# Kernel optimization log

Measured on AMD Instinct MI355X. Metric: run time of the kernel, lower is better.

Reference implementation:

```python
import jax, jax.numpy as jnp
import numpy as np

N_HEADS = 16
N_KV_HEADS = 8
N_REP = 2
HEAD_DIM = 128
SOFTCAP = 50.0
NEG_INF = -2.3819763e38
ROPE_BASE = 10000.0


def _rotate_half(x):
    x1, x2 = jnp.split(x, 2, axis=-1)
    return jnp.concatenate((-x2, x1), axis=-1)


def _rope_cos_sin(seq_len, dtype):
    # Gemma2RotaryEmbedding: inv_freq over even dims, emb = cat(freqs, freqs)
    inv_freq = 1.0 / (ROPE_BASE ** (jnp.arange(0, HEAD_DIM, 2, dtype=jnp.float32) / HEAD_DIM))
    freqs = jnp.arange(seq_len, dtype=jnp.float32)[:, None] * inv_freq[None, :]  # [s, hd/2]
    emb = jnp.concatenate((freqs, freqs), axis=-1)  # [s, hd]
    return jnp.cos(emb).astype(dtype), jnp.sin(emb).astype(dtype)


def setup_inputs() -> dict:
    key = jax.random.key(0)
    ks = jax.random.split(key, 5)
    b, s, d = 2, 2048, 2048
    w_scale = 0.02
    return {
        "x": jax.random.normal(ks[0], (b, s, d), dtype=jnp.float32),
        "wq": jax.random.normal(ks[1], (N_HEADS * HEAD_DIM, d), dtype=jnp.float32) * w_scale,
        "wk": jax.random.normal(ks[2], (N_KV_HEADS * HEAD_DIM, d), dtype=jnp.float32) * w_scale,
        "wv": jax.random.normal(ks[3], (N_KV_HEADS * HEAD_DIM, d), dtype=jnp.float32) * w_scale,
        "wo": jax.random.normal(ks[4], (d, N_HEADS * HEAD_DIM), dtype=jnp.float32) * w_scale,
    }


def reference(x, wq, wk, wv, wo):
    b, s, d = x.shape
    # QKV projections (linear_fn = plain x @ W.T)
    xq = (x @ wq.T).reshape(b, s, N_HEADS, HEAD_DIM).transpose(0, 2, 1, 3)      # [b,h,s,hd]
    xk = (x @ wk.T).reshape(b, s, N_KV_HEADS, HEAD_DIM).transpose(0, 2, 1, 3)   # [b,kv,s,hd]
    xv = (x @ wv.T).reshape(b, s, N_KV_HEADS, HEAD_DIM).transpose(0, 2, 1, 3)
    # Gemma2 rotary on q, k
    cos, sin = _rope_cos_sin(s, x.dtype)  # [s,hd] each, broadcast over b,h
    xq = xq * cos + _rotate_half(xq) * sin
    xk = xk * cos + _rotate_half(xk) * sin
    # repeat_kv: expand kv heads to n_heads
    keys = jnp.repeat(xk, N_REP, axis=1)
    values = jnp.repeat(xv, N_REP, axis=1)
    # scores with scaling and Gemma2 logit softcapping
    scale = float(HEAD_DIM) ** -0.5
    scores = jnp.einsum("bhsd,bhtd->bhst", xq * scale, keys)
    scores = jnp.tanh(scores / SOFTCAP) * SOFTCAP
    # causal additive mask [s, t]
    q_pos = jnp.arange(s)[:, None]
    k_pos = jnp.arange(s)[None, :]
    mask = jnp.where(k_pos <= q_pos, 0.0, NEG_INF).astype(jnp.float32)
    scores = scores + mask  # broadcast over [b,h]
    probs = jax.nn.softmax(scores.astype(jnp.float32), axis=-1).astype(xq.dtype)
    out = jnp.einsum("bhst,bhtd->bhsd", probs, values)
    out = out.transpose(0, 2, 1, 3).reshape(b, s, N_HEADS * HEAD_DIM)
    return out @ wo.T
```

## Files before the change

### kernel.cpp

```cpp
#include <hip/hip_runtime.h>
#include <stdint.h>
#include <stddef.h>

#define S_LEN   2048
#define DMODEL  2048
#define NHEADS  16
#define NKVH    8
#define HD      128
#define QPRE 1.7677669529663688e-3f
#define C1 72.13475204444817f

typedef __attribute__((ext_vector_type(8))) short  short8;
typedef __attribute__((ext_vector_type(4))) float  float4v;

static __device__ __forceinline__ unsigned short f2bf(float f) {
  union { float f; unsigned int u; } v; v.f = f;
  unsigned int u = v.u;
  u += 0x7fffu + ((u >> 16) & 1u);
  return (unsigned short)(u >> 16);
}
static __device__ __forceinline__ float bf2f(unsigned short b) {
  union { unsigned int u; float f; } v; v.u = ((unsigned int)b) << 16;
  return v.f;
}
static __device__ __forceinline__ void gload_lds16(const void* g, void* l) {
  __builtin_amdgcn_global_load_lds(
      (const __attribute__((address_space(1))) void*)g,
      (__attribute__((address_space(3))) void*)l, 16, 0, 0);
}

__global__ __launch_bounds__(256) void cvt_all(
    const float* __restrict__ x,  const float* __restrict__ wq,
    const float* __restrict__ wk, const float* __restrict__ wv,
    const float* __restrict__ wo,
    ushort4* __restrict__ xb, ushort4* __restrict__ wcat,
    ushort4* __restrict__ wob) {
  int i = blockIdx.x * 256 + threadIdx.x;
  const float4* src; ushort4* dst; int j;
  if (i < 2097152)      { src = (const float4*)x;  dst = xb;             j = i; }
  else if (i < 3145728) { src = (const float4*)wq; dst = wcat;           j = i - 2097152; }
  else if (i < 3670016) { src = (const float4*)wk; dst = wcat + 1048576; j = i - 3145728; }
  else if (i < 4194304) { src = (const float4*)wv; dst = wcat + 1572864; j = i - 3670016; }
  else                  { src = (const float4*)wo; dst = wob;            j = i - 4194304; }
  float4 v = src[j];
  ushort4 o;
  o.x = f2bf(v.x); o.y = f2bf(v.y); o.z = f2bf(v.z); o.w = f2bf(v.w);
  dst[j] = o;
}

__global__ __launch_bounds__(256, 2) void gemm_bf16(
    const unsigned short* __restrict__ A,
    const unsigned short* __restrict__ B,
    void* __restrict__ Cout, int N, int mode) {
  const int t    = threadIdx.x;
  const int lane = t & 63;
  const int w    = t >> 6;
  const int l15  = lane & 15;
  const int quad = lane >> 4;
  const int m0   = blockIdx.y * 128;
  const int n0   = blockIdx.x * 128;
  const int wm   = (w >> 1) * 64;
  const int wn   = (w & 1) * 64;

  __shared__ unsigned short At[128 * 32];
  __shared__ unsigned short Bt[128 * 32];

  float4v acc[4][4];
#pragma unroll
  for (int mt = 0; mt < 4; ++mt)
#pragma unroll
    for (int nt = 0; nt < 4; ++nt)
      acc[mt][nt] = (float4v){0.f, 0.f, 0.f, 0.f};

  const unsigned short* Abase = A + (size_t)m0 * DMODEL;
  const unsigned short* Bbase = B + (size_t)n0 * DMODEL;
  const int srow = w * 16 + (lane >> 2);
  const int sch  = (lane & 3) * 8;

  for (int k0 = 0; k0 < DMODEL; k0 += 32) {
#pragma unroll
    for (int r = 0; r < 2; ++r) {
      gload_lds16(Abase + (size_t)(r * 64 + srow) * DMODEL + k0 + sch,
                  At + (r * 256 + w * 64) * 8);
      gload_lds16(Bbase + (size_t)(r * 64 + srow) * DMODEL + k0 + sch,
                  Bt + (r * 256 + w * 64) * 8);
    }
    __syncthreads();
    short8 af[4], bf[4];
#pragma unroll
    for (int mt = 0; mt < 4; ++mt)
      af[mt] = *(const short8*)(At + (wm + mt * 16 + l15) * 32 + quad * 8);
#pragma unroll
    for (int nt = 0; nt < 4; ++nt)
      bf[nt] = *(const short8*)(Bt + (wn + nt * 16 + l15) * 32 + quad * 8);
#pragma unroll
    for (int mt = 0; mt < 4; ++mt)
#pragma unroll
      for (int nt = 0; nt < 4; ++nt)
        acc[mt][nt] = __builtin_amdgcn_mfma_f32_16x16x32_bf16(
            af[mt], bf[nt], acc[mt][nt], 0, 0, 0);
    __syncthreads();
  }

  float* C = (float*)Cout;
#pragma unroll
  for (int mt = 0; mt < 4; ++mt) {
    int row = m0 + wm + mt * 16 + quad * 4;
#pragma unroll
    for (int nt = 0; nt < 4; ++nt) {
      int col = n0 + wn + nt * 16 + l15;
#pragma unroll
      for (int r2 = 0; r2 < 4; ++r2)
        C[(size_t)(row + r2) * N + col] = acc[mt][nt][r2];
    }
  }
}

__global__ __launch_bounds__(512, 2) void gemm256_qkv(
    const unsigned short* __restrict__ A,
    const unsigned short* __restrict__ B,
    unsigned short* __restrict__ C) {
  const int t    = threadIdx.x;
  const int lane = t & 63;
  const int w    = t >> 6;
  const int l15  = lane & 15;
  const int quad = lane >> 4;

  const int id  = blockIdx.x;
  const int swz = (id & 7) * 32 + (id >> 3);
  const int m0  = (swz >> 4) * 256;
  const int n0  = (swz & 15) * 256;

  __shared__ unsigned short sm[2][2][2][128 * 64];

  const int wm  = w >> 2;
  const int wnq = w & 3;
  const int hB  = wnq >> 1;
  const int wnl = (wnq & 1) * 64;

  int soff[2];
#pragma unroll
  for (int i = 0; i < 2; ++i) {
    int P = (w * 2 + i) * 64 + lane;
    int r = P >> 3;
    int lc = (P & 7) ^ (r & 7);
    soff[i] = r * DMODEL + lc * 8;
  }
  const unsigned short* Ab = A + (size_t)m0 * DMODEL;
  const unsigned short* Bb = B + (size_t)n0 * DMODEL;

  auto stage = [&](int mat, int half, int buf, int kt) {
    const unsigned short* g =
        (mat ? Bb : Ab) + (size_t)half * 128 * DMODEL + kt * 64;
    unsigned short* l = &sm[buf][mat][half][(w * 2) * 512];
#pragma unroll
    for (int i = 0; i < 2; ++i)
      gload_lds16(g + soff[i], l + i * 512);
  };

  float4v acc[2][2][4][2];
#pragma unroll
  for (int qm = 0; qm < 2; ++qm)
#pragma unroll
    for (int qn = 0; qn < 2; ++qn)
#pragma unroll
      for (int mt = 0; mt < 4; ++mt)
#pragma unroll
        for (int nt = 0; nt < 2; ++nt)
          acc[qm][qn][mt][nt] = (float4v){0.f, 0.f, 0.f, 0.f};

  stage(0, 0, 0, 0); stage(0, 1, 0, 0); stage(1, 0, 0, 0); stage(1, 1, 0, 0);
  stage(0, 0, 1, 1); stage(0, 1, 1, 1); stage(1, 0, 1, 1);
  asm volatile("s_waitcnt vmcnt(6)" ::: "memory");
  __builtin_amdgcn_s_barrier();

  const int NT = DMODEL / 64;
#pragma unroll 1
  for (int j = 0; j < NT; ++j) {
    const int c = j & 1;
    const unsigned short* As = &sm[c][0][wm][0];
    const unsigned short* Bs = &sm[c][1][hB][0];
    short8 af[4][2], bf0[2][2], bf1[2][2];

#pragma unroll
    for (int mt = 0; mt < 4; ++mt)
#pragma unroll
      for (int kk = 0; kk < 2; ++kk) {
        int r = mt * 16 + l15;
        af[mt][kk] = *(const short8*)&As[r * 64 + (((kk * 4 + quad) ^ (r & 7)) * 8)];
      }
#pragma unroll
    for (int nt = 0; nt < 2; ++nt)
#pragma unroll
      for (int kk = 0; kk < 2; ++kk) {
        int r = wnl + nt * 16 + l15;
        bf0[nt][kk] = *(const short8*)&Bs[r * 64 + (((kk * 4 + quad) ^ (r & 7)) * 8)];
      }
    if (j + 1 < NT) stage(1, 1, c ^ 1, j + 1);
    __builtin_amdgcn_s_barrier();
    __builtin_amdgcn_s_setprio(1);
#pragma unroll
    for (int mt = 0; mt < 4; ++mt)
#pragma unroll
      for (int nt = 0; nt < 2; ++nt)
#pragma unroll
        for (int kk = 0; kk < 2; ++kk)
          acc[0][0][mt][nt] = __builtin_amdgcn_mfma_f32_16x16x32_bf16(
              af[mt][kk], bf0[nt][kk], acc[0][0][mt][nt], 0, 0, 0);
    __builtin_amdgcn_s_setprio(0);
    __builtin_amdgcn_s_barrier();

#pragma unroll
    for (int nt = 0; nt < 2; ++nt)
#pragma unroll
      for (int kk = 0; kk < 2; ++kk) {
        int r = wnl + 32 + nt * 16 + l15;
        bf1[nt][kk] = *(const short8*)&Bs[r * 64 + (((kk * 4 + quad) ^ (r & 7)) * 8)];
      }
    __builtin_amdgcn_s_barrier();
    __builtin_amdgcn_s_setprio(1);
#pragma unroll
    for (int mt = 0; mt < 4; ++mt)
#pragma unroll
      for (int nt = 0; nt < 2; ++nt)
#pragma unroll
        for (int kk = 0; kk < 2; ++kk)
          acc[0][1][mt][nt] = __builtin_amdgcn_mfma_f32_16x16x32_bf16(
              af[mt][kk], bf1[nt][kk], acc[0][1][mt][nt], 0, 0, 0);
    __builtin_amdgcn_s_setprio(0);
    __builtin_amdgcn_s_barrier();

#pragma unroll
    for (int mt = 0; mt < 4; ++mt)
#pragma unroll
      for (int kk = 0; kk < 2; ++kk) {
        int r = 64 + mt * 16 + l15;
        af[mt][kk] = *(const short8*)&As[r * 64 + (((kk * 4 + quad) ^ (r & 7)) * 8)];
      }
    __builtin_amdgcn_s_barrier();
    __builtin_amdgcn_s_setprio(1);
#pragma unroll
    for (int mt = 0; mt < 4; ++mt)
#pragma unroll
      for (int nt = 0; nt < 2; ++nt)
#pragma unroll
        for (int kk = 0; kk < 2; ++kk)
          acc[1][0][mt][nt] = __builtin_amdgcn_mfma_f32_16x16x32_bf16(
              af[mt][kk], bf0[nt][kk], acc[1][0][mt][nt], 0, 0, 0);
    __builtin_amdgcn_s_setprio(0);
    __builtin_amdgcn_s_barrier();

    if (j + 2 < NT) {
      stage(0, 0, c, j + 2); stage(0, 1, c, j + 2); stage(1, 0, c, j + 2);
    }
    __builtin_amdgcn_s_barrier();
    __builtin_amdgcn_s_setprio(1);
#pragma unroll
    for (int mt = 0; mt < 4; ++mt)
#pragma unroll
      for (int nt = 0; nt < 2; ++nt)
#pragma unroll
        for (int kk = 0; kk < 2; ++kk)
          acc[1][1][mt][nt] = __builtin_amdgcn_mfma_f32_16x16x32_bf16(
              af[mt][kk], bf1[nt][kk], acc[1][1][mt][nt], 0, 0, 0);
    __builtin_amdgcn_s_setprio(0);
    if (j + 2 < NT)      { asm volatile("s_waitcnt vmcnt(6)" ::: "memory"); }
    else if (j + 1 < NT) { asm volatile("s_waitcnt vmcnt(0)" ::: "memory"); }
    __builtin_amdgcn_s_barrier();
  }

#pragma unroll
  for (int qm = 0; qm < 2; ++qm)
#pragma unroll
    for (int mt = 0; mt < 4; ++mt) {
      int row0 = m0 + wm * 128 + qm * 64 + mt * 16 + quad * 4;
      int b = row0 >> 11, s0 = row0 & (S_LEN - 1);
#pragma unroll
      for (int qn = 0; qn < 2; ++qn)
#pragma unroll
        for (int nt = 0; nt < 2; ++nt) {
          int col = n0 + wnq * 64 + qn * 32 + nt * 16 + l15;
          float4v v = acc[qm][qn][mt][nt];
          if (col < 2048) {
            int head = col >> 7, d = col & (HD - 1);
#pragma unroll
            for (int r2 = 0; r2 < 4; ++r2)
              C[((size_t)(b * 16 + head) * S_LEN + s0 + r2) * HD + d] = f2bf(v[r2]);
          } else if (col < 3072) {
            int c2 = col - 2048;
            int kvh = c2 >> 7, d = c2 & (HD - 1);
#pragma unroll
            for (int r2 = 0; r2 < 4; ++r2)
              C[8388608 + ((size_t)(b * 8 + kvh) * S_LEN + s0 + r2) * HD + d] = f2bf(v[r2]);
          } else {
            int c2 = col - 3072;
            int kvh = c2 >> 7, d = c2 & (HD - 1);
            ushort4 pk;
            pk.x = f2bf(v[0]); pk.y = f2bf(v[1]);
            pk.z = f2bf(v[2]); pk.w = f2bf(v[3]);
            *(ushort4*)&C[12582912 + ((size_t)(b * 8 + kvh) * HD + d) * S_LEN + s0] = pk;
          }
        }
    }
}

__global__ __launch_bounds__(256) void rope_kernel(unsigned short* __restrict__ Q,
                                                   unsigned short* __restrict__ Kc) {
  int gt = blockIdx.x * 256 + threadIdx.x;
  int r = gt >> 6;
  int j = gt & 63;
  const int QROWS = 2 * NHEADS * S_LEN;
  bool isQ = (r < QROWS);
  unsigned short* p = isQ ? (Q + (size_t)r * HD)
                          : (Kc + (size_t)(r - QROWS) * HD);
  int pos = r & (S_LEN - 1);
  float inv = exp2f(-(float)j * 0.20762050593046868f);
  float ang = (float)pos * inv;
  float c = cosf(ang), s = sinf(ang);
  float sc = isQ ? QPRE : 1.0f;
  float x1 = bf2f(p[j]), x2 = bf2f(p[j + 64]);
  p[j]      = f2bf((x1 * c - x2 * s) * sc);
  p[j + 64] = f2bf((x2 * c + x1 * s) * sc);
}

__global__ __launch_bounds__(256, 2) void attn_kernel(
    const unsigned short* __restrict__ Q,
    const unsigned short* __restrict__ Kc,
    const unsigned short* __restrict__ Vt,
    unsigned short* __restrict__ Aout) {
  const int t    = threadIdx.x;
  const int lane = t & 63;
  const int w    = t >> 6;
  const int l15  = lane & 15;
  const int quad = lane >> 4;
  const int bh = blockIdx.x;
  const int pp = blockIdx.y;
  const int b = bh >> 4, h = bh & 15, kv = h >> 1;
  const int qtA = pp, qtB = 31 - pp;
  const int q0A = qtA * 64, q0B = qtB * 64;
  const int ntB = qtB + 1;

  __shared__ unsigned short Kt[2][64 * 128];
  __shared__ unsigned short Vts[2][128 * 64];
  __shared__ unsigned short Pt[4 * 2 * 1024];

  int offK[4], offV[4];
#pragma unroll
  for (int i = 0; i < 4; ++i) {
    int g = i * 256 + t;
    int rK = g >> 4, cK = (g & 15) ^ (rK & 7);
    offK[i] = rK * HD + cK * 8;
    int rV = g >> 3, cV = (g & 7) ^ (rV & 7);
    offV[i] = rV * S_LEN + cV * 8;
  }

  const unsigned short* QA = Q + ((size_t)(b * NHEADS + h) * S_LEN + q0A + w * 16) * HD;
  const unsigned short* QB = Q + ((size_t)(b * NHEADS + h) * S_LEN + q0B + w * 16) * HD;
  short8 qfA[4], qfB[4];
#pragma unroll
  for (int kk = 0; kk < 4; ++kk) {
    qfA[kk] = *(const short8*)&QA[l15 * HD + kk * 32 + quad * 8];
    qfB[kk] = *(const short8*)&QB[l15 * HD + kk * 32 + quad * 8];
  }

  float4v oA[8], oB[8];
#pragma unroll
  for (int nth = 0; nth < 8; ++nth) {
    oA[nth] = (float4v){0.f, 0.f, 0.f, 0.f};
    oB[nth] = (float4v){0.f, 0.f, 0.f, 0.f};
  }
  float lsA = 0.f, lsB = 0.f;

  const unsigned short* kg0 = Kc + (size_t)(b * NKVH + kv) * S_LEN * HD;
  const unsigned short* vg0 = Vt + (size_t)(b * NKVH + kv) * HD * S_LEN;
  unsigned short* PB = Pt + (w * 2 + 0) * 1024;
  unsigned short* PA = Pt + (w * 2 + 1) * 1024;

  auto stage = [&](int kt, int buf) {
    const unsigned short* kgp = kg0 + (size_t)kt * 64 * HD;
    const unsigned short* vgp = vg0 + (size_t)kt * 64;
#pragma unroll
    for (int i = 0; i < 4; ++i)
      gload_lds16(kgp + offK[i], &Kt[buf][(i * 256 + w * 64) * 8]);
#pragma unroll
    for (int i = 0; i < 4; ++i)
      gload_lds16(vgp + offV[i], &Vts[buf][(i * 256 + w * 64) * 8]);
  };

  auto softcap = [&](float x) -> float {
    float xx = __builtin_amdgcn_fmed3f(x, -0.26f, 0.26f);
    float x2 = xx * xx;
    float u = __builtin_fmaf(0.13333334f, x2, -0.33333334f);
    float v = __builtin_fmaf(u, x2, 1.0f);
    return __builtin_amdgcn_exp2f((C1 * xx) * v);
  };

  stage(0, 0);
  for (int kt = 0; kt < ntB; ++kt) {
    const int cur = kt & 1;
    __syncthreads();
    if (kt + 1 < ntB) stage(kt + 1, cur ^ 1);
    const bool doA   = (kt <= qtA);
    const bool diagA = (kt == qtA);
    const bool diagB = (kt == qtB);
    const unsigned short* Kb = Kt[cur];
    const unsigned short* Vb = Vts[cur];

#pragma unroll
    for (int ntk = 0; ntk < 4; ++ntk) {
      int pb = l15 * 64 + (((ntk * 2 + (quad >> 1)) ^ (l15 & 7)) * 8) + (quad & 1) * 4;
      short8 kf[4];
#pragma unroll
      for (int kk = 0; kk < 4; ++kk)
        kf[kk] = *(const short8*)
            &Kb[(ntk * 16 + l15) * HD + (((kk * 4 + quad) ^ (l15 & 7)) * 8)];

      if (diagB && (ntk * 16 > w * 16 + 15)) {
        uint2 z; z.x = 0u; z.y = 0u;
        *(uint2*)&PB[pb] = z;
      } else {
        float4v s0 = (float4v){0.f, 0.f, 0.f, 0.f};
#pragma unroll
        for (int kk = 0; kk < 4; ++kk)
          s0 = __builtin_amdgcn_mfma_f32_16x16x32_bf16(kf[kk], qfB[kk], s0, 0, 0, 0);
        float pv[4];
#pragma unroll
        for (int r = 0; r < 4; ++r) {
          float p = softcap(s0[r]);
          if (diagB)
            p = (ntk * 16 + quad * 4 + r <= w * 16 + l15) ? p : 0.f;
          lsB += p;
          pv[r] = p;
        }
        union { float f; unsigned u; } u0, u1, u2, u3;
        u0.f = pv[0]; u1.f = pv[1]; u2.f = pv[2]; u3.f = pv[3];
        uint2 pk;
        pk.x = __builtin_amdgcn_perm(u1.u, u0.u, 0x07060302);
        pk.y = __builtin_amdgcn_perm(u3.u, u2.u, 0x07060302);
        *(uint2*)&PB[pb] = pk;
      }

      if (doA) {
        if (diagA && (ntk * 16 > w * 16 + 15)) {
          uint2 z; z.x = 0u; z.y = 0u;
          *(uint2*)&PA[pb] = z;
        } else {
          float4v s0 = (float4v){0.f, 0.f, 0.f, 0.f};
#pragma unroll
          for (int kk = 0; kk < 4; ++kk)
            s0 = __builtin_amdgcn_mfma_f32_16x16x32_bf16(kf[kk], qfA[kk], s0, 0, 0, 0);
          float pv[4];
#pragma unroll
          for (int r = 0; r < 4; ++r) {
            float p = softcap(s0[r]);
            if (diagA)
              p = (ntk * 16 + quad * 4 + r <= w * 16 + l15) ? p : 0.f;
            lsA += p;
            pv[r] = p;
          }
          union { float f; unsigned u; } u0, u1, u2, u3;
          u0.f = pv[0]; u1.f = pv[1]; u2.f = pv[2]; u3.f = pv[3];
          uint2 pk;
          pk.x = __builtin_amdgcn_perm(u1.u, u0.u, 0x07060302);
          pk.y = __builtin_amdgcn_perm(u3.u, u2.u, 0x07060302);
          *(uint2*)&PA[pb] = pk;
        }
      }
    }

#pragma unroll
    for (int kk = 0; kk < 2; ++kk) {
      int sw = ((kk * 4 + quad) ^ (l15 & 7)) * 8;
      short8 pB0 = *(const short8*)&PB[l15 * 64 + sw];
      short8 pA0;
      if (doA) pA0 = *(const short8*)&PA[l15 * 64 + sw];
#pragma unroll
      for (int nth = 0; nth < 8; ++nth) {
        short8 vf = *(const short8*)&Vb[(nth * 16 + l15) * 64 + sw];
        oB[nth] = __builtin_amdgcn_mfma_f32_16x16x32_bf16(pB0, vf, oB[nth], 0, 0, 0);
        if (doA)
          oA[nth] = __builtin_amdgcn_mfma_f32_16x16x32_bf16(pA0, vf, oA[nth], 0, 0, 0);
      }
    }
  }

#pragma unroll
  for (int tile = 0; tile < 2; ++tile) {
    float ls = tile ? lsA : lsB;
    float4v* oo = tile ? oA : oB;
    int q0 = tile ? q0A : q0B;
    float v = ls;
    v += __shfl_xor(v, 16, 64);
    v += __shfl_xor(v, 32, 64);
    float inv = __builtin_amdgcn_rcpf(v);
    float iv[4];
#pragma unroll
    for (int r = 0; r < 4; ++r) iv[r] = __shfl(inv, quad * 4 + r, 64);
    unsigned short* ob = Aout + (size_t)(b * S_LEN + q0 + w * 16) * DMODEL + h * HD;
#pragma unroll
    for (int nth = 0; nth < 8; ++nth) {
#pragma unroll
      for (int r = 0; r < 4; ++r) {
        int row = quad * 4 + r;
        ob[(size_t)row * DMODEL + nth * 16 + l15] = f2bf(oo[nth][r] * iv[r]);
      }
    }
  }
}

extern "C" void kernel_launch(void* const* d_in, const int* in_sizes, int n_in,
                              void* d_out, int out_size, void* d_ws, size_t ws_size,
                              hipStream_t stream) {
  const float* x  = (const float*)d_in[0];
  const float* wq = (const float*)d_in[1];
  const float* wk = (const float*)d_in[2];
  const float* wv = (const float*)d_in[3];
  const float* wo = (const float*)d_in[4];

  char* ws = (char*)d_ws;
  unsigned short* xb   = (unsigned short*)(ws + 0);
  unsigned short* wcat = (unsigned short*)(ws + 16777216);
  unsigned short* wob  = (unsigned short*)(ws + 33554432);
  unsigned short* QKV  = (unsigned short*)(ws + 41943040);
  unsigned short* AO   = (unsigned short*)(ws + 75497472);

  unsigned short* Qw = QKV;
  unsigned short* Kw = QKV + 8388608;
  unsigned short* Vw = QKV + 12582912;

  cvt_all<<<20480, 256, 0, stream>>>(x, wq, wk, wv, wo,
                                     (ushort4*)xb, (ushort4*)wcat, (ushort4*)wob);

  gemm256_qkv<<<256, 512, 0, stream>>>(xb, wcat, QKV);

  rope_kernel<<<24576, 256, 0, stream>>>(Qw, Kw);

  attn_kernel<<<dim3(32, 16), 256, 0, stream>>>(Qw, Kw, Vw, AO);

  gemm_bf16<<<dim3(16, 32), 256, 0, stream>>>(AO, wob, d_out, 2048, 2);
}
```

Before: 323.3 us.

## Split attention key tiles across two wave groups with LDS reduction

The attention block doubles from 256 to 512 threads. Two groups of four waves each take one half of every 64-key tile for the same query rows, and the partial outputs and row sums are then reduced through shared memory before normalisation. The aim is more waves per block, giving better latency hiding and MFMA occupancy, with more causal-mask skipping at 32-key granularity. In exchange it adds a final LDS reduction and barrier, more register pressure under launch_bounds(512,4), and repacks the P scratch into a smaller layout.

```diff
diff --git a/kernel.cpp b/kernel.cpp
--- a/kernel.cpp
+++ b/kernel.cpp
@@ -323,7 +323,7 @@
   p[j + 64] = f2bf((x2 * c + x1 * s) * sc);
 }
 
-__global__ __launch_bounds__(256, 2) void attn_kernel(
+__global__ __launch_bounds__(512, 4) void attn_kernel(
     const unsigned short* __restrict__ Q,
     const unsigned short* __restrict__ Kc,
     const unsigned short* __restrict__ Vt,
@@ -331,6 +331,8 @@
   const int t    = threadIdx.x;
   const int lane = t & 63;
   const int w    = t >> 6;
+  const int g    = w >> 2;
+  const int ws   = w & 3;
   const int l15  = lane & 15;
   const int quad = lane >> 4;
   const int bh = blockIdx.x;
@@ -340,22 +342,23 @@
   const int q0A = qtA * 64, q0B = qtB * 64;
   const int ntB = qtB + 1;
 
-  __shared__ unsigned short Kt[2][64 * 128];
-  __shared__ unsigned short Vts[2][128 * 64];
-  __shared__ unsigned short Pt[4 * 2 * 1024];
-
-  int offK[4], offV[4];
-#pragma unroll
-  for (int i = 0; i < 4; ++i) {
-    int g = i * 256 + t;
-    int rK = g >> 4, cK = (g & 15) ^ (rK & 7);
+  __shared__ unsigned short smem[40960];
+  unsigned short* Pw = smem + 32768 + w * 1024;
+  unsigned short* PB = Pw;
+  unsigned short* PA = Pw + 512;
+
+  int offK[2], offV[2];
+#pragma unroll
+  for (int i = 0; i < 2; ++i) {
+    int gk = i * 512 + t;
+    int rK = gk >> 4, cK = (gk & 15) ^ (rK & 7);
     offK[i] = rK * HD + cK * 8;
-    int rV = g >> 3, cV = (g & 7) ^ (rV & 7);
+    int rV = gk >> 3, cV = (gk & 7) ^ (rV & 7);
     offV[i] = rV * S_LEN + cV * 8;
   }
 
-  const unsigned short* QA = Q + ((size_t)(b * NHEADS + h) * S_LEN + q0A + w * 16) * HD;
-  const unsigned short* QB = Q + ((size_t)(b * NHEADS + h) * S_LEN + q0B + w * 16) * HD;
+  const unsigned short* QA = Q + ((size_t)(b * NHEADS + h) * S_LEN + q0A + ws * 16) * HD;
+  const unsigned short* QB = Q + ((size_t)(b * NHEADS + h) * S_LEN + q0B + ws * 16) * HD;
   short8 qfA[4], qfB[4];
 #pragma unroll
   for (int kk = 0; kk < 4; ++kk) {
@@ -373,18 +376,18 @@
 
   const unsigned short* kg0 = Kc + (size_t)(b * NKVH + kv) * S_LEN * HD;
   const unsigned short* vg0 = Vt + (size_t)(b * NKVH + kv) * HD * S_LEN;
-  unsigned short* PB = Pt + (w * 2 + 0) * 1024;
-  unsigned short* PA = Pt + (w * 2 + 1) * 1024;
 
   auto stage = [&](int kt, int buf) {
     const unsigned short* kgp = kg0 + (size_t)kt * 64 * HD;
     const unsigned short* vgp = vg0 + (size_t)kt * 64;
-#pragma unroll
-    for (int i = 0; i < 4; ++i)
-      gload_lds16(kgp + offK[i], &Kt[buf][(i * 256 + w * 64) * 8]);
-#pragma unroll
-    for (int i = 0; i < 4; ++i)
-      gload_lds16(vgp + offV[i], &Vts[buf][(i * 256 + w * 64) * 8]);
+    unsigned short* kb = smem + buf * 8192;
+    unsigned short* vb = smem + 16384 + buf * 8192;
+#pragma unroll
+    for (int i = 0; i < 2; ++i)
+      gload_lds16(kgp + offK[i], kb + (i * 512 + w * 64) * 8);
+#pragma unroll
+    for (int i = 0; i < 2; ++i)
+      gload_lds16(vgp + offV[i], vb + (i * 512 + w * 64) * 8);
   };
 
   auto softcap = [&](float x) -> float {
@@ -400,61 +403,59 @@
     const int cur = kt & 1;
     __syncthreads();
     if (kt + 1 < ntB) stage(kt + 1, cur ^ 1);
-    const bool doA   = (kt <= qtA);
-    const bool diagA = (kt == qtA);
-    const bool diagB = (kt == qtB);
-    const unsigned short* Kb = Kt[cur];
-    const unsigned short* Vb = Vts[cur];
-
-#pragma unroll
-    for (int ntk = 0; ntk < 4; ++ntk) {
-      int pb = l15 * 64 + (((ntk * 2 + (quad >> 1)) ^ (l15 & 7)) * 8) + (quad & 1) * 4;
-      short8 kf[4];
-#pragma unroll
-      for (int kk = 0; kk < 4; ++kk)
-        kf[kk] = *(const short8*)
-            &Kb[(ntk * 16 + l15) * HD + (((kk * 4 + quad) ^ (l15 & 7)) * 8)];
-
-      if (diagB && (ntk * 16 > w * 16 + 15)) {
-        uint2 z; z.x = 0u; z.y = 0u;
-        *(uint2*)&PB[pb] = z;
-      } else {
-        float4v s0 = (float4v){0.f, 0.f, 0.f, 0.f};
+    const unsigned short* Kb = smem + cur * 8192;
+    const unsigned short* Vb = smem + 16384 + cur * 8192;
+    const int kbase = kt * 64 + g * 32;
+    const int dqB = q0B + ws * 16 - kbase;
+    const int dqA = q0A + ws * 16 - kbase;
+    const bool doB = (dqB >= -15);
+    const bool doA = (dqA >= -15);
+
+#pragma unroll
+    for (int ntk = 0; ntk < 2; ++ntk) {
+      int pb = l15 * 32 + (((ntk * 2 + (quad >> 1)) ^ (l15 & 3)) * 8) + (quad & 1) * 4;
+      const bool actB = doB && (ntk * 16 <= dqB + 15);
+      const bool actA = doA && (ntk * 16 <= dqA + 15);
+      if (doB && !actB) { uint2 z; z.x = 0u; z.y = 0u; *(uint2*)&PB[pb] = z; }
+      if (doA && !actA) { uint2 z; z.x = 0u; z.y = 0u; *(uint2*)&PA[pb] = z; }
+      if (actB || actA) {
+        short8 kf[4];
 #pragma unroll
         for (int kk = 0; kk < 4; ++kk)
-          s0 = __builtin_amdgcn_mfma_f32_16x16x32_bf16(kf[kk], qfB[kk], s0, 0, 0, 0);
-        float pv[4];
-#pragma unroll
-        for (int r = 0; r < 4; ++r) {
-          float p = softcap(s0[r]);
-          if (diagB)
-            p = (ntk * 16 + quad * 4 + r <= w * 16 + l15) ? p : 0.f;
-          lsB += p;
-          pv[r] = p;
+          kf[kk] = *(const short8*)
+              &Kb[(g * 32 + ntk * 16 + l15) * HD + (((kk * 4 + quad) ^ (l15 & 7)) * 8)];
+        if (actB) {
+          float4v s0 = (float4v){0.f, 0.f, 0.f, 0.f};
+#pragma unroll
+          for (int kk = 0; kk < 4; ++kk)
+            s0 = __builtin_amdgcn_mfma_f32_16x16x32_bf16(kf[kk], qfB[kk], s0, 0, 0, 0);
+          const bool part = (ntk * 16 + 15 > dqB);
+          float pv[4];
+#pragma unroll
+          for (int r = 0; r < 4; ++r) {
+            float p = softcap(s0[r]);
+            if (part) p = (ntk * 16 + quad * 4 + r <= dqB + l15) ? p : 0.f;
+            lsB += p;
+            pv[r] = p;
+          }
+          union { float f; unsigned u; } u0, u1, u2, u3;
+          u0.f = pv[0]; u1.f = pv[1]; u2.f = pv[2]; u3.f = pv[3];
+          uint2 pk;
+          pk.x = __builtin_amdgcn_perm(u1.u, u0.u, 0x07060302);
+          pk.y = __builtin_amdgcn_perm(u3.u, u2.u, 0x07060302);
+          *(uint2*)&PB[pb] = pk;
         }
-        union { float f; unsigned u; } u0, u1, u2, u3;
-        u0.f = pv[0]; u1.f = pv[1]; u2.f = pv[2]; u3.f = pv[3];
-        uint2 pk;
-        pk.x = __builtin_amdgcn_perm(u1.u, u0.u, 0x07060302);
-        pk.y = __builtin_amdgcn_perm(u3.u, u2.u, 0x07060302);
-        *(uint2*)&PB[pb] = pk;
-      }
-
-      if (doA) {
-        if (diagA && (ntk * 16 > w * 16 + 15)) {
-          uint2 z; z.x = 0u; z.y = 0u;
-          *(uint2*)&PA[pb] = z;
-        } else {
+        if (actA) {
           float4v s0 = (float4v){0.f, 0.f, 0.f, 0.f};
 #pragma unroll
           for (int kk = 0; kk < 4; ++kk)
             s0 = __builtin_amdgcn_mfma_f32_16x16x32_bf16(kf[kk], qfA[kk], s0, 0, 0, 0);
+          const bool part = (ntk * 16 + 15 > dqA);
           float pv[4];
 #pragma unroll
           for (int r = 0; r < 4; ++r) {
             float p = softcap(s0[r]);
-            if (diagA)
-              p = (ntk * 16 + quad * 4 + r <= w * 16 + l15) ? p : 0.f;
+            if (part) p = (ntk * 16 + quad * 4 + r <= dqA + l15) ? p : 0.f;
             lsA += p;
             pv[r] = p;
           }
@@ -468,41 +469,62 @@
       }
     }
 
-#pragma unroll
-    for (int kk = 0; kk < 2; ++kk) {
-      int sw = ((kk * 4 + quad) ^ (l15 & 7)) * 8;
-      short8 pB0 = *(const short8*)&PB[l15 * 64 + sw];
-      short8 pA0;
-      if (doA) pA0 = *(const short8*)&PA[l15 * 64 + sw];
+    if (doB || doA) {
+      short8 pB0, pA0;
+      if (doB) pB0 = *(const short8*)&PB[l15 * 32 + ((quad ^ (l15 & 3)) * 8)];
+      if (doA) pA0 = *(const short8*)&PA[l15 * 32 + ((quad ^ (l15 & 3)) * 8)];
 #pragma unroll
       for (int nth = 0; nth < 8; ++nth) {
-        short8 vf = *(const short8*)&Vb[(nth * 16 + l15) * 64 + sw];
-        oB[nth] = __builtin_amdgcn_mfma_f32_16x16x32_bf16(pB0, vf, oB[nth], 0, 0, 0);
-        if (doA)
-          oA[nth] = __builtin_amdgcn_mfma_f32_16x16x32_bf16(pA0, vf, oA[nth], 0, 0, 0);
-      }
-    }
-  }
-
-#pragma unroll
-  for (int tile = 0; tile < 2; ++tile) {
-    float ls = tile ? lsA : lsB;
-    float4v* oo = tile ? oA : oB;
-    int q0 = tile ? q0A : q0B;
-    float v = ls;
-    v += __shfl_xor(v, 16, 64);
-    v += __shfl_xor(v, 32, 64);
-    float inv = __builtin_amdgcn_rcpf(v);
-    float iv[4];
-#pragma unroll
-    for (int r = 0; r < 4; ++r) iv[r] = __shfl(inv, quad * 4 + r, 64);
-    unsigned short* ob = Aout + (size_t)(b * S_LEN + q0 + w * 16) * DMODEL + h * HD;
+        short8 vf = *(const short8*)
+            &Vb[(nth * 16 + l15) * 64 + (((g * 4 + quad) ^ (l15 & 7)) * 8)];
+        if (doB) oB[nth] = __builtin_amdgcn_mfma_f32_16x16x32_bf16(pB0, vf, oB[nth], 0, 0, 0);
+        if (doA) oA[nth] = __builtin_amdgcn_mfma_f32_16x16x32_bf16(pA0, vf, oA[nth], 0, 0, 0);
+      }
+    }
+  }
+
+  __syncthreads();
+  float* oscr = (float*)smem;
+  float* lscr = (float*)(smem + 32768);
+  if (g == 1) {
 #pragma unroll
     for (int nth = 0; nth < 8; ++nth) {
-#pragma unroll
-      for (int r = 0; r < 4; ++r) {
-        int row = quad * 4 + r;
-        ob[(size_t)row * DMODEL + nth * 16 + l15] = f2bf(oo[nth][r] * iv[r]);
+      *(float4v*)&oscr[ws * 4096 + (0 * 8 + nth) * 256 + lane * 4] = oB[nth];
+      *(float4v*)&oscr[ws * 4096 + (1 * 8 + nth) * 256 + lane * 4] = oA[nth];
+    }
+    lscr[ws * 128 + lane] = lsB;
+    lscr[ws * 128 + 64 + lane] = lsA;
+  }
+  __syncthreads();
+  if (g == 0) {
+#pragma unroll
+    for (int nth = 0; nth < 8; ++nth) {
+      oB[nth] += *(const float4v*)&oscr[ws * 4096 + (0 * 8 + nth) * 256 + lane * 4];
+      oA[nth] += *(const float4v*)&oscr[ws * 4096 + (1 * 8 + nth) * 256 + lane * 4];
+    }
+    lsB += lscr[ws * 128 + lane];
+    lsA += lscr[ws * 128 + 64 + lane];
+
+#pragma unroll
+    for (int tile = 0; tile < 2; ++tile) {
+      float ls = tile ? lsA : lsB;
+      float4v* oo = tile ? oA : oB;
+      int q0 = tile ? q0A : q0B;
+      float v = ls;
+      v += __shfl_xor(v, 16, 64);
+      v += __shfl_xor(v, 32, 64);
+      float inv = __builtin_amdgcn_rcpf(v);
+      float iv[4];
+#pragma unroll
+      for (int r = 0; r < 4; ++r) iv[r] = __shfl(inv, quad * 4 + r, 64);
+      unsigned short* ob = Aout + (size_t)(b * S_LEN + q0 + ws * 16) * DMODEL + h * HD;
+#pragma unroll
+      for (int nth = 0; nth < 8; ++nth) {
+#pragma unroll
+        for (int r = 0; r < 4; ++r) {
+          int row = quad * 4 + r;
+          ob[(size_t)row * DMODEL + nth * 16 + l15] = f2bf(oo[nth][r] * iv[r]);
+        }
       }
     }
   }
@@ -535,7 +557,7 @@
 
   rope_kernel<<<24576, 256, 0, stream>>>(Qw, Kw);
 
-  attn_kernel<<<dim3(32, 16), 256, 0, stream>>>(Qw, Kw, Vw, AO);
+  attn_kernel<<<dim3(32, 16), 512, 0, stream>>>(Qw, Kw, Vw, AO);
 
   gemm_bf16<<<dim3(16, 32), 256, 0, stream>>>(AO, wob, d_out, 2048, 2);
 }
```

New measurement: 427.6 us. 32.3% more time.
